# Performance work log

Hardware: AMD Instinct MI355X
Metric: run time of the kernel (lower is better)

## Reference

```python
import jax, jax.numpy as jnp
import numpy as np

PI = float(np.pi)


def _conv2d(x, w, b, pad):
    out = jax.lax.conv_general_dilated(x, w, (1, 1), ((pad, pad), (pad, pad)),
                                       dimension_numbers=('NCHW', 'OIHW', 'NCHW'))
    return out + b[None, :, None, None]


def _group_norm(x, gamma, beta, groups, eps=1e-5):
    B, C, h, w = x.shape
    xg = x.reshape(B, groups, C // groups, h, w)
    mu = xg.mean(axis=(2, 3, 4), keepdims=True)
    var = xg.var(axis=(2, 3, 4), keepdims=True)
    xn = ((xg - mu) / jnp.sqrt(var + eps)).reshape(B, C, h, w)
    return xn * gamma[None, :, None, None] + beta[None, :, None, None]


def _l2n(x, eps=1e-12):
    return x / jnp.maximum(jnp.linalg.norm(x, axis=1, keepdims=True), eps)


def _dense_sift(x):
    # kornia DenseSIFTDescriptor defaults: 8 ang bins, 4x4 spatial bins,
    # spatial_bin_size=4, rootsift=True, clipval=0.2, stride=1, padding=1
    eps = 1e-10
    NA = 8
    # 'diff' spatial gradient with replicate padding, normalized (/2)
    xp = jnp.pad(x, ((0, 0), (0, 0), (1, 1), (1, 1)), mode='edge')
    gx = (xp[:, :, 1:-1, 2:] - xp[:, :, 1:-1, :-2]) * 0.5
    gy = (xp[:, :, 2:, 1:-1] - xp[:, :, :-2, 1:-1]) * 0.5
    mag = jnp.sqrt(gx * gx + gy * gy + eps)[:, 0]           # [B,H,W]
    ori = jnp.arctan2(gy, gx + eps)[:, 0] + 2.0 * PI
    o_big = NA * ori / (2.0 * PI)
    bo0f = jnp.floor(o_big)
    wo1_ = o_big - bo0f
    wo0 = (1.0 - wo1_) * mag
    wo1 = wo1_ * mag
    bo0 = bo0f.astype(jnp.int32) % NA
    bo1 = (bo0 + 1) % NA
    bins = jnp.arange(NA).reshape(1, NA, 1, 1)
    ang = ((bo0[:, None] == bins).astype(x.dtype) * wo0[:, None]
           + (bo1[:, None] == bins).astype(x.dtype) * wo1[:, None])  # [B,8,H,W]
    # SIFT pooling kernel ksize=4 (triangle weights), conv pad=2 -> H+1,W+1
    xc2 = np.array([0.5, 1.5, 1.5, 0.5], np.float32)
    pool1 = np.outer(xc2, xc2) / 4.0
    pk = jnp.asarray(np.tile(pool1[None, None], (NA, 1, 1, 1)))  # depthwise [8,1,4,4]
    pooled = jax.lax.conv_general_dilated(ang, pk, (1, 1), ((2, 2), (2, 2)),
                dimension_numbers=('NCHW', 'OIHW', 'NCHW'), feature_group_count=NA)
    # identity reshape conv: 128 = 8 ang * 4*4 spatial bins, pad=1 -> back to H,W
    rk = jnp.asarray(np.eye(128, dtype=np.float32).reshape(128, NA, 4, 4))
    out = jax.lax.conv_general_dilated(pooled, rk, (1, 1), ((1, 1), (1, 1)),
                dimension_numbers=('NCHW', 'OIHW', 'NCHW'))
    out = jnp.clip(_l2n(out), 0.0, 0.2)
    out = _l2n(out)
    l1 = jnp.maximum(jnp.sum(jnp.abs(out), axis=1, keepdims=True), 1e-12)
    return jnp.sqrt(out / l1 + eps)  # rootsift


def _joint_bilateral(x, guide, ksize=5, sigma_color=0.1, sigma_space=1.5):
    pad = ksize // 2
    ax = np.arange(ksize, dtype=np.float32) - ksize // 2
    g1 = np.exp(-ax ** 2 / (2.0 * sigma_space ** 2))
    g1 = g1 / g1.sum()
    sk = np.outer(g1, g1)  # normalized 5x5 gaussian space kernel
    xp = jnp.pad(x, ((0, 0), (0, 0), (pad, pad), (pad, pad)), mode='reflect')
    gp = jnp.pad(guide, ((0, 0), (0, 0), (pad, pad), (pad, pad)), mode='reflect')
    h, w = x.shape[2], x.shape[3]
    inv = -0.5 / (sigma_color ** 2)
    num = jnp.zeros_like(x)
    den = jnp.zeros((x.shape[0], 1, h, w), x.dtype)
    for dy in range(ksize):           # fixed 5x5 tap loop, accumulated in-place
        for dx in range(ksize):
            gs = gp[:, :, dy:dy + h, dx:dx + w]
            cd = jnp.sum(jnp.abs(gs - guide), axis=1, keepdims=True) ** 2  # l1 squared
            wgt = sk[dy, dx] * jnp.exp(inv * cd)
            num = num + wgt * xp[:, :, dy:dy + h, dx:dx + w]
            den = den + wgt
    return num / den


def _forward(x, gt, w1, b1, g1w, g1b, w2, b2, g2w, g2b, w3, b3, g3w, g3b,
             w4, b4, g4w, g4b, w5, b5):
    orig = x
    f = _dense_sift(x)
    f = jax.nn.relu(_group_norm(_conv2d(f, w1, b1, 2), g1w, g1b, 8))
    f = jax.nn.relu(_group_norm(_conv2d(f, w2, b2, 1), g2w, g2b, 8))
    f = jax.nn.relu(_group_norm(_conv2d(f, w3, b3, 1), g3w, g3b, 4))
    f = jax.nn.relu(_group_norm(_conv2d(f, w4, b4, 1), g4w, g4b, 4))
    f = _conv2d(f, w5, b5, 1)
    # rgb_to_yuv(gt)[:, 1:] as guidance
    r, g, b = gt[:, 0], gt[:, 1], gt[:, 2]
    u = -0.147 * r - 0.289 * g + 0.436 * b
    v = 0.615 * r - 0.515 * g - 0.100 * b
    guide = jnp.stack([u, v], axis=1)
    f = _joint_bilateral(f, guide)

    def _rescale(c, lo, hi):
        c = (c - c.min()) / (c.max() - c.min() + 1e-6)  # global min/max over B,H,W
        c = jnp.clip(c, 0.0, 1.0)
        return c * (hi - lo) + lo

    U = _rescale(f[:, 0], -0.436, 0.436)
    V = _rescale(f[:, 1], -0.615, 0.615)
    Y = orig[:, 0]
    R = Y + 1.14 * V
    G = Y - 0.396 * U - 0.581 * V
    B = Y + 2.029 * U
    return jnp.stack([R, G, B], axis=1)


def setup_inputs() -> dict:
    key = jax.random.key(0)
    ks = jax.random.split(key, 16)
    B = 4
    d = {
        'x': jax.random.uniform(ks[0], (B, 1, 270, 512), jnp.float32),
        'gt': jax.random.uniform(ks[1], (B, 3, 270, 512), jnp.float32),
        'w1': jax.random.normal(ks[2], (64, 128, 5, 5), jnp.float32) * 0.02,
        'b1': jnp.zeros((64,), jnp.float32),
        'g1w': jnp.ones((64,), jnp.float32), 'g1b': jnp.zeros((64,), jnp.float32),
        'w2': jax.random.normal(ks[3], (32, 64, 3, 3), jnp.float32) * 0.04,
        'b2': jnp.zeros((32,), jnp.float32),
        'g2w': jnp.ones((32,), jnp.float32), 'g2b': jnp.zeros((32,), jnp.float32),
        'w3': jax.random.normal(ks[4], (16, 32, 3, 3), jnp.float32) * 0.05,
        'b3': jnp.zeros((16,), jnp.float32),
        'g3w': jnp.ones((16,), jnp.float32), 'g3b': jnp.zeros((16,), jnp.float32),
        'w4': jax.random.normal(ks[5], (8, 16, 3, 3), jnp.float32) * 0.08,
        'b4': jnp.zeros((8,), jnp.float32),
        'g4w': jnp.ones((8,), jnp.float32), 'g4b': jnp.zeros((8,), jnp.float32),
        'w5': jax.random.normal(ks[6], (2, 8, 3, 3), jnp.float32) * 0.1,
        'b5': jnp.zeros((2,), jnp.float32),
    }
    return d


def reference(x, gt, w1, b1, g1w, g1b, w2, b2, g2w, g2b, w3, b3, g3w, g3b,
              w4, b4, g4w, g4b, w5, b5):
    return _forward(x, gt, w1, b1, g1w, g1b, w2, b2, g2w, g2b, w3, b3, g3w, g3b,
                    w4, b4, g4w, g4b, w5, b5)
```

## Files before the change

kernel.cpp:

```cpp
#include <hip/hip_runtime.h>

constexpr int NB  = 4;
constexpr int IH  = 270;
constexpr int IW  = 512;
constexpr int NPIX = IH * IW;
constexpr int PH  = 271;
constexpr int PW  = 513;
constexpr float TWO_PI_F = 6.28318530717958647692f;

typedef short  bf16x8 __attribute__((ext_vector_type(8)));
typedef float floatx4 __attribute__((ext_vector_type(4)));

__device__ inline unsigned short f2bf(float x) {
  union { float f; unsigned u; } un; un.f = x;
  unsigned r = un.u + 0x7fff + ((un.u >> 16) & 1);
  return (unsigned short)(r >> 16);
}
__device__ inline float bf2f(unsigned short u) {
  union { unsigned u; float f; } x; x.u = ((unsigned)u) << 16; return x.f;
}
__device__ inline unsigned fkey(float f) {
  unsigned u = __float_as_uint(f);
  return (u & 0x80000000u) ? ~u : (u | 0x80000000u);
}
__device__ inline float funkey(unsigned k) {
  unsigned u = (k & 0x80000000u) ? (k ^ 0x80000000u) : ~k;
  return __uint_as_float(u);
}
__device__ inline void gn_coef_thread(const float* __restrict__ stats,
                                      const float* __restrict__ gamma,
                                      const float* __restrict__ beta,
                                      float* cA, float* cB, int C, int chper, int b) {
  int c = threadIdx.x;
  if (c < C) {
    int g0 = (c / chper) * chper;
    float S = 0.f, S2 = 0.f;
    for (int k = 0; k < chper; k++) {
      S  += stats[(b * C + g0 + k) * 2];
      S2 += stats[(b * C + g0 + k) * 2 + 1];
    }
    double Nd = (double)chper * NPIX;
    double mu = (double)S / Nd;
    double var = (double)S2 / Nd - mu * mu;
    double rstd = 1.0 / sqrt(var + 1e-5);
    float A = (float)rstd * gamma[c];
    cA[c] = A;
    cB[c] = beta[c] - (float)mu * A;
  }
}

__device__ inline void mfma_pack_one(const float* __restrict__ w, short* __restrict__ wB,
                                     int i, int CO, int CI, int KK, int CHUNKS) {
  int j = i & 7, l = (i >> 3) & 63, f = i >> 9;
  int t = f % KK; int fc = f / KK; int cc = fc % CHUNKS; int g = fc / CHUNKS;
  int ci = cc * 32 + ((l >> 4) << 3) + j;
  int co = g * 16 + (l & 15);
  float v = (ci < CI && co < CO) ? w[((size_t)co * CI + ci) * KK + t] : 0.f;
  wB[i] = (short)f2bf(v);
}
__device__ inline void repack_one(const float* __restrict__ w, float* __restrict__ wT,
                                  int i, int CO, int CI, int KK) {
  int o = i / (CI * KK);
  int r = i % (CI * KK);
  int ci = r / KK, kk = r % KK;
  wT[(kk * CI + ci) * CO + o] = w[i];
}
__global__ __launch_bounds__(256) void prep_kernel(
    const float* __restrict__ w1, const float* __restrict__ w2,
    const float* __restrict__ w3, const float* __restrict__ w4,
    const float* __restrict__ w5,
    short* __restrict__ w1B, short* __restrict__ w2B, short* __restrict__ w3B,
    float* __restrict__ w4T, float* __restrict__ w5T) {
  constexpr int N1 = 4 * 4 * 25 * 512;
  constexpr int N2 = 2 * 2 * 9 * 512;
  constexpr int N3 = 1 * 1 * 9 * 512;
  constexpr int N4 = 8 * 16 * 9;
  constexpr int N5 = 2 * 8 * 9;
  int i = blockIdx.x * 256 + threadIdx.x;
  if (i < N1) { mfma_pack_one(w1, w1B, i, 64, 128, 25, 4); return; }
  i -= N1;
  if (i < N2) { mfma_pack_one(w2, w2B, i, 32, 64, 9, 2); return; }
  i -= N2;
  if (i < N3) { mfma_pack_one(w3, w3B, i, 16, 32, 9, 1); return; }
  i -= N3;
  if (i < N4) { repack_one(w4, w4T, i, 8, 16, 9); return; }
  i -= N4;
  if (i < N5) { repack_one(w5, w5T, i, 2, 8, 9); return; }
}

__global__ __launch_bounds__(256) void sift_desc_kernel(
    const float* __restrict__ x, short* __restrict__ descg) {
  const int b = blockIdx.z;
  const int x0 = blockIdx.x * 16, y0 = blockIdx.y * 16;
  __shared__ float xs[24][25];
  __shared__ float wo0[22][23], wo1[22][23];
  __shared__ int   bo0[22][23];
  __shared__ float pooled[8][19][20];
  __shared__ float s1s[256], gs[256];
  const int tid = threadIdx.x;
  const float* xb = x + (size_t)b * NPIX;

  for (int t = tid; t < 576; t += 256) {
    int r = t / 24, c = t % 24;
    int gy = min(max(y0 - 4 + r, 0), IH - 1);
    int gx = min(max(x0 - 4 + c, 0), IW - 1);
    xs[r][c] = xb[gy * IW + gx];
  }
  __syncthreads();

  for (int t = tid; t < 484; t += 256) {
    int r = t / 22, c = t % 22;
    int gy = y0 - 3 + r, gx = x0 - 3 + c;
    float w0 = 0.f, w1v = 0.f; int b0 = 0;
    if (gy >= 0 && gy < IH && gx >= 0 && gx < IW) {
      float gxv = (xs[r + 1][c + 2] - xs[r + 1][c]) * 0.5f;
      float gyv = (xs[r + 2][c + 1] - xs[r][c + 1]) * 0.5f;
      float mag = sqrtf(gxv * gxv + gyv * gyv + 1e-10f);
      float ori = atan2f(gyv, gxv + 1e-10f) + TWO_PI_F;
      float obig = ori * (8.0f / TWO_PI_F);
      float bf = floorf(obig);
      float w1_ = obig - bf;
      w0  = (1.0f - w1_) * mag;
      w1v = w1_ * mag;
      b0  = ((int)bf) & 7;
    }
    wo0[r][c] = w0; wo1[r][c] = w1v; bo0[r][c] = b0;
  }
  __syncthreads();

  const float pwt[4] = {0.25f, 0.75f, 0.75f, 0.25f};
  for (int t = tid; t < 361; t += 256) {
    int pr = t / 19, pc = t % 19;
    int py = y0 - 1 + pr, px = x0 - 1 + pc;
    float acc[8] = {0, 0, 0, 0, 0, 0, 0, 0};
    if (py >= 0 && py < PH && px >= 0 && px < PW) {
      #pragma unroll
      for (int i = 0; i < 4; i++) {
        #pragma unroll
        for (int j = 0; j < 4; j++) {
          float w0 = wo0[pr + i][pc + j], w1v = wo1[pr + i][pc + j];
          int b0 = bo0[pr + i][pc + j];
          int b1i = (b0 + 1) & 7;
          float pw = pwt[i] * pwt[j];
          #pragma unroll
          for (int a = 0; a < 8; a++) {
            float add = (a == b0 ? w0 : 0.f) + (a == b1i ? w1v : 0.f);
            acc[a] = fmaf(pw, add, acc[a]);
          }
        }
      }
    }
    #pragma unroll
    for (int a = 0; a < 8; a++) pooled[a][pr][pc] = acc[a];
  }
  __syncthreads();

  {
    int py = tid >> 4, px = tid & 15;
    int y = y0 + py;
    float s1 = 0.f, g = 0.f;
    if (y < IH) {
      float sum2 = 0.f;
      for (int c = 0; c < 128; c++) {
        int a = c >> 4, i = (c >> 2) & 3, j = c & 3;
        float p = pooled[a][py + i][px + j];
        sum2 = fmaf(p, p, sum2);
      }
      s1 = 1.0f / fmaxf(sqrtf(sum2), 1e-12f);
      float st2 = 0.f, st = 0.f;
      for (int c = 0; c < 128; c++) {
        int a = c >> 4, i = (c >> 2) & 3, j = c & 3;
        float p = pooled[a][py + i][px + j];
        float tv = fminf(p * s1, 0.2f);
        st2 = fmaf(tv, tv, st2);
        st += tv;
      }
      float s2 = 1.0f / fmaxf(sqrtf(st2), 1e-12f);
      float l1 = fmaxf(s2 * st, 1e-12f);
      g = s2 / l1;
    }
    s1s[tid] = s1; gs[tid] = g;
  }
  __syncthreads();

  for (int k = 0; k < 16; k++) {
    int gidx = k * 256 + tid;
    int cc = gidx >> 10, pix = (gidx >> 2) & 255, sub = gidx & 3;
    int py = pix >> 4, px = pix & 15;
    int y = y0 + py;
    if (y >= IH) continue;
    float s1v = s1s[pix], gv = gs[pix];
    int a = cc * 2 + (sub >> 1);
    unsigned short v8[8];
    #pragma unroll
    for (int jj = 0; jj < 8; jj++) {
      int i = (sub * 2 + (jj >> 2)) & 3;
      int j = jj & 3;
      float p = pooled[a][py + i][px + j];
      v8[jj] = f2bf(sqrtf(fminf(p * s1v, 0.2f) * gv + 1e-10f));
    }
    uint4 pk;
    pk.x = (unsigned)v8[0] | ((unsigned)v8[1] << 16);
    pk.y = (unsigned)v8[2] | ((unsigned)v8[3] << 16);
    pk.z = (unsigned)v8[4] | ((unsigned)v8[5] << 16);
    pk.w = (unsigned)v8[6] | ((unsigned)v8[7] << 16);
    size_t base = ((size_t)(b * 4 + cc) * NPIX + (size_t)y * IW + (x0 + px)) * 32 + sub * 8;
    *(uint4*)(descg + base) = pk;
  }
}

__global__ __launch_bounds__(256, 2) void conv1_mfma_kernel(
    const short* __restrict__ descg, const short* __restrict__ w1B,
    const float* __restrict__ bias, unsigned short* __restrict__ out,
    float* __restrict__ stats) {
  const int b = blockIdx.z;
  const int x0 = blockIdx.x * 16, y0 = blockIdx.y * 16;
  __shared__ __align__(16) char smem_raw[33408];
  short* desc = (short*)smem_raw;
  float* cout = (float*)smem_raw;

  const int tid = threadIdx.x;
  const int wave = tid >> 6, lane = tid & 63;
  const int quad = lane >> 4, lm = lane & 15;

  floatx4 acc[4][4];
  #pragma unroll
  for (int n = 0; n < 4; n++)
    #pragma unroll
    for (int i = 0; i < 4; i++) acc[n][i] = (floatx4){0.f, 0.f, 0.f, 0.f};

  for (int cc = 0; cc < 4; cc++) {
    __syncthreads();
    const short* dg = descg + (size_t)(b * 4 + cc) * NPIX * 32;
    for (int u = tid; u < 1600; u += 256) {
      int pos = u >> 2, sub = u & 3;
      int r = pos / 20, c = pos % 20;
      int gy = y0 - 2 + r, gx = x0 - 2 + c;
      uint4 val = {0u, 0u, 0u, 0u};
      if (gy >= 0 && gy < IH && gx >= 0 && gx < IW)
        val = *(const uint4*)(dg + ((size_t)gy * IW + gx) * 32 + sub * 8);
      *(uint4*)(desc + pos * 40 + sub * 8) = val;
    }
    __syncthreads();

    const short* wb = w1B + (size_t)cc * 25 * 512 + (lane << 3);
    bf16x8 bfrC[4], avC[4], bfrN[4], avN[4];
    #pragma unroll
    for (int n = 0; n < 4; n++)
      bfrN[n] = *(const bf16x8*)(wb + (size_t)n * 4 * 25 * 512);
    #pragma unroll
    for (int i = 0; i < 4; i++)
      avN[i] = *(const bf16x8*)(desc + ((wave * 4 + i) * 20 + lm) * 40 + quad * 8);
    #pragma unroll
    for (int t = 0; t < 25; t++) {
      #pragma unroll
      for (int n = 0; n < 4; n++) bfrC[n] = bfrN[n];
      #pragma unroll
      for (int i = 0; i < 4; i++) avC[i] = avN[i];
      if (t < 24) {
        int t1 = t + 1, ky1 = t1 / 5, kx1 = t1 % 5;
        #pragma unroll
        for (int n = 0; n < 4; n++)
          bfrN[n] = *(const bf16x8*)(wb + ((size_t)n * 4 * 25 + t1) * 512);
        #pragma unroll
        for (int i = 0; i < 4; i++)
          avN[i] = *(const bf16x8*)(desc + ((wave * 4 + i + ky1) * 20 + lm + kx1) * 40 + quad * 8);
      }
      #pragma unroll
      for (int n = 0; n < 4; n++)
        #pragma unroll
        for (int i = 0; i < 4; i++)
          acc[n][i] = __builtin_amdgcn_mfma_f32_16x16x32_bf16(avC[i], bfrC[n], acc[n][i], 0, 0, 0);
    }
  }

  unsigned short* ob = out + (size_t)b * 64 * NPIX;
  for (int h = 0; h < 2; h++) {
    __syncthreads();
    #pragma unroll
    for (int nn = 0; nn < 2; nn++)
      #pragma unroll
      for (int i = 0; i < 4; i++)
        #pragma unroll
        for (int r = 0; r < 4; r++)
          cout[(nn * 16 + lm) * 261 + (wave * 4 + i) * 16 + quad * 4 + r] = acc[h * 2 + nn][i][r];
    __syncthreads();
    for (int v = tid; v < 8192; v += 256) {
      int col = v >> 8, px = v & 255;
      int y = y0 + (px >> 4), x = x0 + (px & 15);
      if (y < IH)
        ob[(size_t)(h * 32 + col) * NPIX + y * IW + x] = f2bf(cout[col * 261 + px] + bias[h * 32 + col]);
    }
    int col = tid >> 3, seg = tid & 7;
    int co = h * 32 + col;
    float bv = bias[co];
    float sum = 0.f, sq = 0.f;
    #pragma unroll
    for (int rr = 0; rr < 2; rr++) {
      int row = seg * 2 + rr;
      if (y0 + row < IH) {
        #pragma unroll
        for (int k = 0; k < 16; k++) {
          float vv = cout[col * 261 + row * 16 + k] + bv;
          sum += vv; sq += vv * vv;
        }
      }
    }
    sum += __shfl_down(sum, 4); sq += __shfl_down(sq, 4);
    sum += __shfl_down(sum, 2); sq += __shfl_down(sq, 2);
    sum += __shfl_down(sum, 1); sq += __shfl_down(sq, 1);
    if ((tid & 7) == 0) {
      atomicAdd(&stats[(b * 64 + co) * 2], sum);
      atomicAdd(&stats[(b * 64 + co) * 2 + 1], sq);
    }
  }
}

template <int CI, int CO, int CHPER, bool STATS>
__global__ __launch_bounds__(256) void convk3_mfma_kernel(
    const unsigned short* __restrict__ xin, const short* __restrict__ wB,
    const float* __restrict__ bias, const float* __restrict__ statsIn,
    const float* __restrict__ gamma, const float* __restrict__ beta,
    float* __restrict__ statsOut, unsigned short* __restrict__ out) {
  constexpr int CHUNKS = CI / 32;
  constexpr int G = CO / 16;
  constexpr int MPW = 2 * G;
  constexpr int CIS = CI + 8;
  constexpr int TILE_B = 180 * CIS * 2;
  constexpr int COUT_B = CO * 133 * 4;
  constexpr int UNION_B = TILE_B > COUT_B ? TILE_B : COUT_B;
  __shared__ __align__(16) char sm[UNION_B + CI * 8];
  short* tile = (short*)sm;
  float* cout = (float*)sm;
  float* cA = (float*)(sm + UNION_B);
  float* cB = cA + CI;

  const int b = blockIdx.z;
  const int x0 = blockIdx.x * 16, y0 = blockIdx.y * 8;
  const int tid = threadIdx.x;
  const int wave = tid >> 6, lane = tid & 63;
  const int quad = lane >> 4, lm = lane & 15;
  const int n = wave % G, mh = wave / G;

  gn_coef_thread(statsIn, gamma, beta, cA, cB, CI, CHPER, b);
  __syncthreads();

  const unsigned short* xb = xin + (size_t)b * CI * NPIX;
  for (int v = tid; v < (CI / 2) * 180; v += 256) {
    int cp = v / 180, pos = v % 180;
    int r = pos / 18, c = pos % 18;
    int gy = y0 - 1 + r, gx = x0 - 1 + c;
    float v0 = 0.f, v1 = 0.f;
    if (gy >= 0 && gy < IH && gx >= 0 && gx < IW) {
      v0 = fmaxf(fmaf(bf2f(xb[(size_t)(2 * cp) * NPIX + gy * IW + gx]), cA[2 * cp], cB[2 * cp]), 0.f);
      v1 = fmaxf(fmaf(bf2f(xb[(size_t)(2 * cp + 1) * NPIX + gy * IW + gx]), cA[2 * cp + 1], cB[2 * cp + 1]), 0.f);
    }
    unsigned pk = (unsigned)f2bf(v0) | ((unsigned)f2bf(v1) << 16);
    *(unsigned*)(tile + pos * CIS + 2 * cp) = pk;
  }
  __syncthreads();

  floatx4 acc[MPW];
  #pragma unroll
  for (int i = 0; i < MPW; i++) acc[i] = (floatx4){0.f, 0.f, 0.f, 0.f};

  constexpr int NT = CHUNKS * 9;
  const short* wbase = wB + ((size_t)n * NT) * 512 + (lane << 3);
  bf16x8 bfrC, avC[MPW], bfrN, avN[MPW];
  bfrN = *(const bf16x8*)(wbase);
  #pragma unroll
  for (int i = 0; i < MPW; i++)
    avN[i] = *(const bf16x8*)(tile + ((mh * MPW + i) * 18 + lm) * CIS + quad * 8);
  #pragma unroll
  for (int t = 0; t < NT; t++) {
    bfrC = bfrN;
    #pragma unroll
    for (int i = 0; i < MPW; i++) avC[i] = avN[i];
    if (t < NT - 1) {
      int t1 = t + 1;
      int cc1 = t1 / 9, r1 = t1 % 9, ky1 = r1 / 3, kx1 = r1 % 3;
      bfrN = *(const bf16x8*)(wbase + (size_t)t1 * 512);
      #pragma unroll
      for (int i = 0; i < MPW; i++)
        avN[i] = *(const bf16x8*)(tile + ((mh * MPW + i + ky1) * 18 + lm + kx1) * CIS + cc1 * 32 + quad * 8);
    }
    #pragma unroll
    for (int i = 0; i < MPW; i++)
      acc[i] = __builtin_amdgcn_mfma_f32_16x16x32_bf16(avC[i], bfrC, acc[i], 0, 0, 0);
  }
  __syncthreads();
  #pragma unroll
  for (int i = 0; i < MPW; i++) {
    #pragma unroll
    for (int r = 0; r < 4; r++) {
      int pixel = (mh * MPW + i) * 16 + quad * 4 + r;
      cout[(n * 16 + lm) * 133 + pixel] = acc[i][r];
    }
  }
  __syncthreads();
  unsigned short* ob = out + (size_t)b * CO * NPIX;
  for (int v = tid; v < CO * 128; v += 256) {
    int co = v >> 7, px = v & 127;
    int y = y0 + (px >> 4), x = x0 + (px & 15);
    if (y < IH) ob[(size_t)co * NPIX + y * IW + x] = f2bf(cout[co * 133 + px] + bias[co]);
  }
  if (STATS) {
    constexpr int TPC = 256 / CO;
    constexpr int PXT = 128 / TPC;
    int col = tid / TPC, seg = tid % TPC;
    float bv = bias[col];
    float sum = 0.f, sq = 0.f;
    #pragma unroll
    for (int k = 0; k < PXT; k++) {
      int p = seg * PXT + k;
      if (y0 + (p >> 4) < IH) {
        float vv = cout[col * 133 + p] + bv;
        sum += vv; sq += vv * vv;
      }
    }
    #pragma unroll
    for (int off = TPC / 2; off > 0; off >>= 1) {
      sum += __shfl_down(sum, off);
      sq  += __shfl_down(sq, off);
    }
    if (seg == 0) {
      atomicAdd(&statsOut[(b * CO + col) * 2], sum);
      atomicAdd(&statsOut[(b * CO + col) * 2 + 1], sq);
    }
  }
}

template <int CI, int CO, int CHPER, bool STATS, bool OUT_BF16>
__global__ __launch_bounds__(256) void convs_kernel(
    const unsigned short* __restrict__ xin, const float* __restrict__ wT,
    const float* __restrict__ bias, const float* __restrict__ statsIn,
    const float* __restrict__ gamma, const float* __restrict__ beta,
    float* __restrict__ statsOut, void* __restrict__ outv) {
  constexpr int OPT = CO / 2;
  const int b = blockIdx.z;
  const int x0 = blockIdx.x * 16, y0 = blockIdx.y * 8;
  __shared__ float tile[CI * 180];
  __shared__ float cA[CI], cB[CI];
  __shared__ float ssum[CO], ssq[CO];
  gn_coef_thread(statsIn, gamma, beta, cA, cB, CI, CHPER, b);
  if (STATS && threadIdx.x < CO) { ssum[threadIdx.x] = 0.f; ssq[threadIdx.x] = 0.f; }
  __syncthreads();
  const unsigned short* xb = xin + (size_t)b * CI * NPIX;
  for (int t = threadIdx.x; t < CI * 180; t += 256) {
    int ci = t / 180, rc = t % 180, r = rc / 18, c = rc % 18;
    int gy = y0 - 1 + r, gx = x0 - 1 + c;
    float v = 0.f;
    if (gy >= 0 && gy < IH && gx >= 0 && gx < IW)
      v = fmaxf(fmaf(bf2f(xb[(size_t)ci * NPIX + gy * IW + gx]), cA[ci], cB[ci]), 0.f);
    tile[t] = v;
  }
  __syncthreads();
  const int t = threadIdx.x;
  const int px = t & 127, og = t >> 7;
  const int pyy = px >> 4, pxx = px & 15;
  const int oc0 = og * OPT;
  const int y = y0 + pyy, x = x0 + pxx;
  float acc[OPT] = {};
  for (int ky = 0; ky < 3; ky++) {
    for (int kx = 0; kx < 3; kx++) {
      const float* wrow = wT + (size_t)((ky * 3 + kx) * CI) * CO + oc0;
      for (int ci = 0; ci < CI; ci++) {
        float v = tile[ci * 180 + (pyy + ky) * 18 + pxx + kx];
        #pragma unroll
        for (int o = 0; o < OPT; o++) acc[o] = fmaf(v, wrow[ci * CO + o], acc[o]);
      }
    }
  }
  if (y < IH) {
    #pragma unroll
    for (int o = 0; o < OPT; o++) {
      float vv = acc[o] + bias[oc0 + o];
      if (OUT_BF16) {
        unsigned short* ob = (unsigned short*)outv + (size_t)b * CO * NPIX;
        ob[(size_t)(oc0 + o) * NPIX + y * IW + x] = f2bf(vv);
      } else {
        float* ob = (float*)outv + (size_t)b * CO * NPIX;
        ob[(size_t)(oc0 + o) * NPIX + y * IW + x] = vv;
      }
      if (STATS) {
        atomicAdd(&ssum[oc0 + o], vv);
        atomicAdd(&ssq[oc0 + o], vv * vv);
      }
    }
  }
  if (STATS) {
    __syncthreads();
    if (threadIdx.x < CO) {
      atomicAdd(&statsOut[(b * CO + threadIdx.x) * 2], ssum[threadIdx.x]);
      atomicAdd(&statsOut[(b * CO + threadIdx.x) * 2 + 1], ssq[threadIdx.x]);
    }
  }
}

__global__ __launch_bounds__(256) void bilateral_kernel(
    const float* __restrict__ f, const float* __restrict__ gt,
    float* __restrict__ out, unsigned* __restrict__ mmbits) {
  const int b = blockIdx.z;
  const int x0 = blockIdx.x * 16, y0 = blockIdx.y * 16;
  __shared__ float gu[20][20], gv[20][20], f0s[20][20], f1s[20][20];
  __shared__ float red[4][4];
  const float* gtb = gt + (size_t)b * 3 * NPIX;
  const float* fb = f + (size_t)b * 2 * NPIX;
  for (int t = threadIdx.x; t < 400; t += 256) {
    int r = t / 20, c = t % 20;
    int gy = y0 - 2 + r, gx = x0 - 2 + c;
    if (gy < 0) gy = -gy;
    if (gy > IH - 1) gy = 2 * (IH - 1) - gy;
    if (gx < 0) gx = -gx;
    if (gx > IW - 1) gx = 2 * (IW - 1) - gx;
    int p = gy * IW + gx;
    float rr = gtb[p], gg = gtb[NPIX + p], bb = gtb[2 * NPIX + p];
    gu[r][c]  = -0.147f * rr - 0.289f * gg + 0.436f * bb;
    gv[r][c]  =  0.615f * rr - 0.515f * gg - 0.100f * bb;
    f0s[r][c] = fb[p];
    f1s[r][c] = fb[NPIX + p];
  }
  __syncthreads();
  const int t = threadIdx.x;
  const int lx = t % 16, ly = t / 16;
  const int y = y0 + ly, x = x0 + lx;
  const bool valid = (y < IH);

  float o0 = 0.f, o1 = 0.f;
  if (valid) {
    float g1v[5];
    float s = 0.f;
    #pragma unroll
    for (int k = 0; k < 5; k++) {
      float a = (float)(k - 2);
      g1v[k] = expf(-a * a / 4.5f);
      s += g1v[k];
    }
    #pragma unroll
    for (int k = 0; k < 5; k++) g1v[k] /= s;
    float cu = gu[ly + 2][lx + 2], cv = gv[ly + 2][lx + 2];
    float num0 = 0.f, num1 = 0.f, den = 0.f;
    #pragma unroll
    for (int dy = 0; dy < 5; dy++) {
      #pragma unroll
      for (int dx = 0; dx < 5; dx++) {
        float du = fabsf(gu[ly + dy][lx + dx] - cu) + fabsf(gv[ly + dy][lx + dx] - cv);
        float wgt = g1v[dy] * g1v[dx] * expf(-50.0f * du * du);
        num0 = fmaf(wgt, f0s[ly + dy][lx + dx], num0);
        num1 = fmaf(wgt, f1s[ly + dy][lx + dx], num1);
        den += wgt;
      }
    }
    o0 = num0 / den; o1 = num1 / den;
    float* ob = out + (size_t)b * 2 * NPIX;
    ob[y * IW + x] = o0;
    ob[NPIX + y * IW + x] = o1;
  }
  float mn0 = valid ? o0 : 1e30f,  mx0 = valid ? o0 : -1e30f;
  float mn1 = valid ? o1 : 1e30f,  mx1 = valid ? o1 : -1e30f;
  #pragma unroll
  for (int off = 32; off > 0; off >>= 1) {
    mn0 = fminf(mn0, __shfl_xor(mn0, off));
    mx0 = fmaxf(mx0, __shfl_xor(mx0, off));
    mn1 = fminf(mn1, __shfl_xor(mn1, off));
    mx1 = fmaxf(mx1, __shfl_xor(mx1, off));
  }
  if ((t & 63) == 0) {
    red[t >> 6][0] = mn0; red[t >> 6][1] = mx0;
    red[t >> 6][2] = mn1; red[t >> 6][3] = mx1;
  }
  __syncthreads();
  if (t == 0) {
    for (int w = 1; w < 4; w++) {
      red[0][0] = fminf(red[0][0], red[w][0]);
      red[0][1] = fmaxf(red[0][1], red[w][1]);
      red[0][2] = fminf(red[0][2], red[w][2]);
      red[0][3] = fmaxf(red[0][3], red[w][3]);
    }
    atomicMax(&mmbits[0], fkey(red[0][1]));
    atomicMax(&mmbits[1], fkey(red[0][3]));
    atomicMin(&mmbits[2], fkey(red[0][0]));
    atomicMin(&mmbits[3], fkey(red[0][2]));
  }
}

__global__ __launch_bounds__(256) void final_kernel(
    const float* __restrict__ bil, const float* __restrict__ x,
    const unsigned* __restrict__ mmbits, float* __restrict__ out) {
  int i = blockIdx.x * 256 + threadIdx.x;
  if (i >= NB * NPIX) return;
  float mx0 = funkey(mmbits[0]), mx1 = funkey(mmbits[1]);
  float mn0 = funkey(mmbits[2]), mn1 = funkey(mmbits[3]);
  int b = i / NPIX, p = i % NPIX;
  float f0 = bil[(size_t)b * 2 * NPIX + p];
  float f1 = bil[(size_t)b * 2 * NPIX + NPIX + p];
  float U = (f0 - mn0) / (mx0 - mn0 + 1e-6f);
  U = fminf(fmaxf(U, 0.f), 1.f) * 0.872f - 0.436f;
  float V = (f1 - mn1) / (mx1 - mn1 + 1e-6f);
  V = fminf(fmaxf(V, 0.f), 1.f) * 1.23f - 0.615f;
  float Y = x[(size_t)b * NPIX + p];
  float* ob = out + (size_t)b * 3 * NPIX;
  ob[p]            = Y + 1.14f * V;
  ob[NPIX + p]     = Y - 0.396f * U - 0.581f * V;
  ob[2 * NPIX + p] = Y + 2.029f * U;
}

extern "C" void kernel_launch(void* const* d_in, const int* in_sizes, int n_in,
                              void* d_out, int out_size, void* d_ws, size_t ws_size,
                              hipStream_t stream) {
  const float* x   = (const float*)d_in[0];
  const float* gt  = (const float*)d_in[1];
  const float* w1  = (const float*)d_in[2];
  const float* b1  = (const float*)d_in[3];
  const float* g1w = (const float*)d_in[4];
  const float* g1b = (const float*)d_in[5];
  const float* w2  = (const float*)d_in[6];
  const float* b2  = (const float*)d_in[7];
  const float* g2w = (const float*)d_in[8];
  const float* g2b = (const float*)d_in[9];
  const float* w3  = (const float*)d_in[10];
  const float* b3  = (const float*)d_in[11];
  const float* g3w = (const float*)d_in[12];
  const float* g3b = (const float*)d_in[13];
  const float* w4  = (const float*)d_in[14];
  const float* b4  = (const float*)d_in[15];
  const float* g4w = (const float*)d_in[16];
  const float* g4b = (const float*)d_in[17];
  const float* w5  = (const float*)d_in[18];
  const float* b5  = (const float*)d_in[19];
  float* out = (float*)d_out;

  char* ws = (char*)d_ws;
  float* stats1 = (float*)ws;
  float* stats2 = stats1 + 512;
  float* stats3 = stats2 + 256;
  float* stats4 = stats3 + 128;
  unsigned* mmbits = (unsigned*)(ws + 12288);
  char* base = ws + 16384;
  short* descg = (short*)base;
  size_t descg_shorts = (size_t)NB * 4 * NPIX * 32;
  unsigned short* bufB_h = (unsigned short*)base;
  float* c5    = (float*)(base + 36000000);
  float* bilat = (float*)(base + 41000000);
  short* w1B = descg + descg_shorts;
  short* w2B = w1B + 204800;
  short* w3B = w2B + 18432;
  float* w4T = (float*)(w3B + 4608);
  float* w5T = w4T + 1152;
  unsigned short* bufA_h = (unsigned short*)(w5T + 144);

  hipMemsetAsync(ws, 0, 12304, stream);
  hipMemsetAsync(ws + 12296, 0xFF, 8, stream);

  prep_kernel<<<896, 256, 0, stream>>>(w1, w2, w3, w4, w5, w1B, w2B, w3B, w4T, w5T);

  sift_desc_kernel<<<dim3(32, 17, NB), 256, 0, stream>>>(x, descg);

  conv1_mfma_kernel<<<dim3(32, 17, NB), 256, 0, stream>>>(descg, w1B, b1, bufA_h, stats1);

  convk3_mfma_kernel<64, 32, 8, true><<<dim3(32, 34, NB), 256, 0, stream>>>(
      bufA_h, w2B, b2, stats1, g1w, g1b, stats2, bufB_h);

  convk3_mfma_kernel<32, 16, 4, true><<<dim3(32, 34, NB), 256, 0, stream>>>(
      bufB_h, w3B, b3, stats2, g2w, g2b, stats3, bufA_h);

  convs_kernel<16, 8, 4, true, true><<<dim3(32, 34, NB), 256, 0, stream>>>(
      bufA_h, w4T, b4, stats3, g3w, g3b, stats4, bufB_h);

  convs_kernel<8, 2, 2, false, false><<<dim3(32, 34, NB), 256, 0, stream>>>(
      bufB_h, w5T, b5, stats4, g4w, g4b, nullptr, c5);

  bilateral_kernel<<<dim3(32, 17, NB), 256, 0, stream>>>(c5, gt, bilat, mmbits);
  final_kernel<<<(NB * NPIX + 255) / 256, 256, 0, stream>>>(bilat, x, mmbits, out);

  (void)in_sizes; (void)n_in; (void)out_size; (void)ws_size;
}
```

Baseline: 1.265 ms.

## Split conv1 MFMA work across 8 waves with halved output channels per wave

Conv1 now runs with 512 threads per block, with each wave computing two of the four output-channel groups for four rows instead of all four groups. This halves the accumulator registers per wave and drops the software-pipelined A-fragment prefetch, aiming for higher occupancy and more waves to hide latency. The trade-off is that each descriptor tile fragment is read from LDS by two waves, and the weight prefetch is kept while LDS loads are no longer double-buffered. The epilogue and statistics reduction are remapped to the wider block, using 16-lane shuffles.

```diff
diff --git a/kernel.cpp b/kernel.cpp
--- a/kernel.cpp
+++ b/kernel.cpp
@@ -209,7 +209,7 @@
   }
 }
 
-__global__ __launch_bounds__(256, 2) void conv1_mfma_kernel(
+__global__ __launch_bounds__(512, 4) void conv1_mfma_kernel(
     const short* __restrict__ descg, const short* __restrict__ w1B,
     const float* __restrict__ bias, unsigned short* __restrict__ out,
     float* __restrict__ stats) {
@@ -222,17 +222,18 @@
   const int tid = threadIdx.x;
   const int wave = tid >> 6, lane = tid & 63;
   const int quad = lane >> 4, lm = lane & 15;
-
-  floatx4 acc[4][4];
+  const int nh = wave & 1, mh = wave >> 1;
+
+  floatx4 acc[2][4];
   #pragma unroll
-  for (int n = 0; n < 4; n++)
-    #pragma unroll
-    for (int i = 0; i < 4; i++) acc[n][i] = (floatx4){0.f, 0.f, 0.f, 0.f};
+  for (int j = 0; j < 2; j++)
+    #pragma unroll
+    for (int i = 0; i < 4; i++) acc[j][i] = (floatx4){0.f, 0.f, 0.f, 0.f};
 
   for (int cc = 0; cc < 4; cc++) {
     __syncthreads();
     const short* dg = descg + (size_t)(b * 4 + cc) * NPIX * 32;
-    for (int u = tid; u < 1600; u += 256) {
+    for (int u = tid; u < 1600; u += 512) {
       int pos = u >> 2, sub = u & 3;
       int r = pos / 20, c = pos % 20;
       int gy = y0 - 2 + r, gx = x0 - 2 + c;
@@ -244,72 +245,68 @@
     __syncthreads();
 
     const short* wb = w1B + (size_t)cc * 25 * 512 + (lane << 3);
-    bf16x8 bfrC[4], avC[4], bfrN[4], avN[4];
-    #pragma unroll
-    for (int n = 0; n < 4; n++)
-      bfrN[n] = *(const bf16x8*)(wb + (size_t)n * 4 * 25 * 512);
-    #pragma unroll
-    for (int i = 0; i < 4; i++)
-      avN[i] = *(const bf16x8*)(desc + ((wave * 4 + i) * 20 + lm) * 40 + quad * 8);
+    bf16x8 bfrC[2], bfrN[2];
+    #pragma unroll
+    for (int j = 0; j < 2; j++)
+      bfrN[j] = *(const bf16x8*)(wb + (size_t)(nh * 2 + j) * 100 * 512);
     #pragma unroll
     for (int t = 0; t < 25; t++) {
-      #pragma unroll
-      for (int n = 0; n < 4; n++) bfrC[n] = bfrN[n];
-      #pragma unroll
-      for (int i = 0; i < 4; i++) avC[i] = avN[i];
+      int ky = t / 5, kx = t % 5;
+      #pragma unroll
+      for (int j = 0; j < 2; j++) bfrC[j] = bfrN[j];
       if (t < 24) {
-        int t1 = t + 1, ky1 = t1 / 5, kx1 = t1 % 5;
+        int t1 = t + 1;
         #pragma unroll
-        for (int n = 0; n < 4; n++)
-          bfrN[n] = *(const bf16x8*)(wb + ((size_t)n * 4 * 25 + t1) * 512);
+        for (int j = 0; j < 2; j++)
+          bfrN[j] = *(const bf16x8*)(wb + ((size_t)(nh * 2 + j) * 100 + t1) * 512);
+      }
+      bf16x8 av[4];
+      #pragma unroll
+      for (int i = 0; i < 4; i++)
+        av[i] = *(const bf16x8*)(desc + ((mh * 4 + i + ky) * 20 + lm + kx) * 40 + quad * 8);
+      #pragma unroll
+      for (int j = 0; j < 2; j++)
         #pragma unroll
         for (int i = 0; i < 4; i++)
-          avN[i] = *(const bf16x8*)(desc + ((wave * 4 + i + ky1) * 20 + lm + kx1) * 40 + quad * 8);
-      }
-      #pragma unroll
-      for (int n = 0; n < 4; n++)
-        #pragma unroll
-        for (int i = 0; i < 4; i++)
-          acc[n][i] = __builtin_amdgcn_mfma_f32_16x16x32_bf16(avC[i], bfrC[n], acc[n][i], 0, 0, 0);
+          acc[j][i] = __builtin_amdgcn_mfma_f32_16x16x32_bf16(av[i], bfrC[j], acc[j][i], 0, 0, 0);
     }
   }
 
   unsigned short* ob = out + (size_t)b * 64 * NPIX;
   for (int h = 0; h < 2; h++) {
     __syncthreads();
-    #pragma unroll
-    for (int nn = 0; nn < 2; nn++)
-      #pragma unroll
-      for (int i = 0; i < 4; i++)
+    if (nh == h) {
+      #pragma unroll
+      for (int j = 0; j < 2; j++)
         #pragma unroll
-        for (int r = 0; r < 4; r++)
-          cout[(nn * 16 + lm) * 261 + (wave * 4 + i) * 16 + quad * 4 + r] = acc[h * 2 + nn][i][r];
+        for (int i = 0; i < 4; i++)
+          #pragma unroll
+          for (int r = 0; r < 4; r++)
+            cout[(j * 16 + lm) * 261 + (mh * 4 + i) * 16 + quad * 4 + r] = acc[j][i][r];
+    }
     __syncthreads();
-    for (int v = tid; v < 8192; v += 256) {
+    for (int v = tid; v < 8192; v += 512) {
       int col = v >> 8, px = v & 255;
       int y = y0 + (px >> 4), x = x0 + (px & 15);
       if (y < IH)
         ob[(size_t)(h * 32 + col) * NPIX + y * IW + x] = f2bf(cout[col * 261 + px] + bias[h * 32 + col]);
     }
-    int col = tid >> 3, seg = tid & 7;
+    int col = tid >> 4, seg = tid & 15;
     int co = h * 32 + col;
     float bv = bias[co];
     float sum = 0.f, sq = 0.f;
-    #pragma unroll
-    for (int rr = 0; rr < 2; rr++) {
-      int row = seg * 2 + rr;
-      if (y0 + row < IH) {
-        #pragma unroll
-        for (int k = 0; k < 16; k++) {
-          float vv = cout[col * 261 + row * 16 + k] + bv;
-          sum += vv; sq += vv * vv;
-        }
-      }
-    }
-    sum += __shfl_down(sum, 4); sq += __shfl_down(sq, 4);
-    sum += __shfl_down(sum, 2); sq += __shfl_down(sq, 2);
-    sum += __shfl_down(sum, 1); sq += __shfl_down(sq, 1);
-    if ((tid & 7) == 0) {
+    if (y0 + seg < IH) {
+      #pragma unroll
+      for (int k = 0; k < 16; k++) {
+        float vv = cout[col * 261 + seg * 16 + k] + bv;
+        sum += vv; sq += vv * vv;
+      }
+    }
+    sum += __shfl_down(sum, 8, 16); sq += __shfl_down(sq, 8, 16);
+    sum += __shfl_down(sum, 4, 16); sq += __shfl_down(sq, 4, 16);
+    sum += __shfl_down(sum, 2, 16); sq += __shfl_down(sq, 2, 16);
+    sum += __shfl_down(sum, 1, 16); sq += __shfl_down(sq, 1, 16);
+    if (seg == 0) {
       atomicAdd(&stats[(b * 64 + co) * 2], sum);
       atomicAdd(&stats[(b * 64 + co) * 2 + 1], sq);
     }
@@ -656,7 +653,7 @@
 
   sift_desc_kernel<<<dim3(32, 17, NB), 256, 0, stream>>>(x, descg);
 
-  conv1_mfma_kernel<<<dim3(32, 17, NB), 256, 0, stream>>>(descg, w1B, b1, bufA_h, stats1);
+  conv1_mfma_kernel<<<dim3(32, 17, NB), 512, 0, stream>>>(descg, w1B, b1, bufA_h, stats1);
 
   convk3_mfma_kernel<64, 32, 8, true><<<dim3(32, 34, NB), 256, 0, stream>>>(
       bufA_h, w2B, b2, stats1, g1w, g1b, stats2, bufB_h);
```

Result: slower. 1.482 ms (+17.2%).
